# Performance work log

Measured on AMD Instinct MI355X. Metric: run time of the kernel, lower is better.

## Reference

```python
import jax, jax.numpy as jnp
import numpy as np

EPS = 1e-8


def setup_inputs() -> dict:
    key = jax.random.key(0)
    ks = jax.random.split(key, 8)
    B, N, D = 8, 2048, 768
    H, R = 768, 4
    return {
        "x": jax.random.normal(ks[0], (B, N, D), dtype=jnp.float32),
        "scale": jnp.ones((D,), dtype=jnp.float32),
        "U": jax.random.normal(ks[1], (H, R), dtype=jnp.float32) * 0.02,
        "V": jax.random.normal(ks[2], (H, R), dtype=jnp.float32) * 0.02,
        "S_param": jax.random.normal(ks[3], (H, H), dtype=jnp.float32) * 0.01,
        "Bm": jax.random.normal(ks[4], (H, D), dtype=jnp.float32) * (1.0 / np.sqrt(D)),
        "Cm": jax.random.normal(ks[5], (D, H), dtype=jnp.float32) * (1.0 / np.sqrt(H)),
        "gate_w": jax.random.normal(ks[6], (D, D), dtype=jnp.float32) * (1.0 / np.sqrt(D)),
        "gate_b": jnp.zeros((D,), dtype=jnp.float32),
        "alpha": jnp.full((1,), 0.1, dtype=jnp.float32),
    }


def reference(x, scale, U, V, S_param, Bm, Cm, gate_w, gate_b, alpha):
    B, N, D = x.shape
    H = Bm.shape[0]
    # A = diag(A_diag) + U V^T + (S - S^T); A_diag is a fixed buffer.
    A_diag = -jnp.linspace(1.0, float(H), H, dtype=x.dtype) / H
    A = jnp.diag(A_diag) + U @ V.T + (S_param - S_param.T)
    At = A.T  # apply as h @ A.T
    # RMSNorm
    rms = jnp.sqrt(jnp.mean(x * x, axis=-1, keepdims=True) + EPS)
    xn = x / rms * scale
    # Precompute input injections u_t = x_t @ B.T for all t: (N, B, H)
    u = jnp.einsum('bnd,hd->nbh', xn, Bm)

    def step(h, ut):
        h = h @ At + ut
        return h, h @ Cm.T  # (B, D)

    h0 = jnp.zeros((B, H), dtype=x.dtype)
    _, y_fwd = jax.lax.scan(step, h0, u)                 # (N, B, D)
    _, y_bwd = jax.lax.scan(step, h0, u, reverse=True)   # (N, B, D), indexed in time order
    y = 0.5 * (y_fwd + y_bwd)
    y = jnp.swapaxes(y, 0, 1)  # (B, N, D)
    # Gate
    g = jax.nn.sigmoid(jnp.einsum('bnd,ed->bne', xn, gate_w) + gate_b)
    y = y * g
    # Skip (dropout is identity in eval)
    return x + alpha * y
```

## Files before the change

kernel.cpp:

```cpp
#include <hip/hip_runtime.h>


typedef short  bfrag __attribute__((ext_vector_type(8)));
typedef float  ffrag __attribute__((ext_vector_type(4)));
typedef float  f4    __attribute__((ext_vector_type(4)));
typedef short  s4v   __attribute__((ext_vector_type(4)));

#define DEV static __device__ __forceinline__
#define Hn 768
#define FLS 132

DEV unsigned short f2bf(float f) {
  unsigned u = __float_as_uint(f);
  u += 0x7fffu + ((u >> 16) & 1u);
  return (unsigned short)(u >> 16);
}
DEV float bf2f(unsigned short s) { return __uint_as_float(((unsigned)s) << 16); }

DEV ffrag mfma16(bfrag a, bfrag b, ffrag c) {
  return __builtin_amdgcn_mfma_f32_16x16x32_bf16(a, b, c, 0, 0, 0);
}

DEV void glds16(const unsigned short* g, unsigned short* l) {
  __builtin_amdgcn_global_load_lds(
      (const __attribute__((address_space(1))) unsigned int*)g,
      (__attribute__((address_space(3))) unsigned int*)l, 16, 0, 0);
}

template<int N> DEV void vwait() {
  if constexpr (N == 0)       asm volatile("s_waitcnt vmcnt(0)" ::: "memory");
  else if constexpr (N == 4)  asm volatile("s_waitcnt vmcnt(4)" ::: "memory");
  else if constexpr (N == 6)  asm volatile("s_waitcnt vmcnt(6)" ::: "memory");
  else if constexpr (N == 8)  asm volatile("s_waitcnt vmcnt(8)" ::: "memory");
  else if constexpr (N == 12) asm volatile("s_waitcnt vmcnt(12)" ::: "memory");
}

union BF8 { bfrag v; unsigned short u[8]; };

__global__ __launch_bounds__(256) void k_abuild(
    const float* __restrict__ U, const float* __restrict__ V,
    const float* __restrict__ S, const float* __restrict__ Bm,
    const float* __restrict__ Cm, const float* __restrict__ gw,
    float* __restrict__ Af, float* __restrict__ AfT,
    unsigned short* __restrict__ Abf,
    unsigned short* __restrict__ Bmb, unsigned short* __restrict__ Cmb,
    unsigned short* __restrict__ gwb, unsigned short* __restrict__ zp) {
  int i = blockIdx.x;
  int task = blockIdx.y;
  if (task == 0) {
    float u0 = U[i*4+0], u1 = U[i*4+1], u2 = U[i*4+2], u3 = U[i*4+3];
    for (int j = threadIdx.x; j < Hn; j += 256) {
      float a = u0*V[j*4+0] + u1*V[j*4+1] + u2*V[j*4+2] + u3*V[j*4+3]
              + S[i*Hn+j] - S[j*Hn+i];
      if (i == j) a += -(float)(i+1) / 768.0f;
      Af[i*Hn+j]  = a;
      AfT[j*Hn+i] = a;
      Abf[i*Hn+j] = f2bf(a);
    }
    if (i == 0) for (int j = threadIdx.x; j < 1024; j += 256) zp[j] = 0;
  } else {
    const float* src = (task==1) ? Bm : (task==2) ? Cm : gw;
    unsigned short* dst = (task==1) ? Bmb : (task==2) ? Cmb : gwb;
    for (int j = threadIdx.x; j < Hn; j += 256) dst[i*Hn+j] = f2bf(src[i*Hn+j]);
  }
}

__global__ __launch_bounds__(256) void k_rms(
    const float* __restrict__ x, const float* __restrict__ scale,
    unsigned short* __restrict__ xn) {
  int row  = blockIdx.x * 4 + (threadIdx.x >> 6);
  int lane = threadIdx.x & 63;
  int b = row >> 11, t = row & 2047;
  const float* xr = x + (long)row * Hn;
  float v[12];
  float ss = 0.f;
#pragma unroll
  for (int j = 0; j < 12; ++j) { v[j] = xr[lane + j*64]; ss += v[j]*v[j]; }
#pragma unroll
  for (int off = 1; off < 64; off <<= 1) ss += __shfl_xor(ss, off);
  float inv = 1.0f / sqrtf(ss / 768.0f + 1e-8f);
  unsigned short* dst = xn + ((long)t * 8 + b) * Hn;
#pragma unroll
  for (int j = 0; j < 12; ++j) dst[lane + j*64] = f2bf(v[j] * inv * scale[lane + j*64]);
}

__global__ __launch_bounds__(512) void k_sq(
    const float* __restrict__ X, const float* __restrict__ XT,
    float* __restrict__ Z, float* __restrict__ ZT,
    unsigned short* __restrict__ Zbf) {
  int tid = threadIdx.x, lane = tid & 63, w = tid >> 6;
  int mw = w >> 2, nw = w & 3, l15 = lane & 15, lhi = lane >> 4;
  int rb = blockIdx.x * 64, cb = blockIdx.y * 128;
  ffrag acc[2][2] = {};
  for (int kt = 0; kt < 24; ++kt) {
    int k0 = kt*32 + lhi*8;
    BF8 ah[2], al[2], bh[2], bl[2];
#pragma unroll
    for (int mt = 0; mt < 2; ++mt) {
      const f4* p = (const f4*)(X + (long)(rb + mw*32 + mt*16 + l15) * Hn + k0);
      f4 x0 = p[0], x1 = p[1];
#pragma unroll
      for (int j = 0; j < 8; ++j) {
        float f = (j < 4) ? x0[j] : x1[j-4];
        unsigned short h = f2bf(f);
        ah[mt].u[j] = h; al[mt].u[j] = f2bf(f - bf2f(h));
      }
    }
#pragma unroll
    for (int nt = 0; nt < 2; ++nt) {
      const f4* p = (const f4*)(XT + (long)(cb + nw*32 + nt*16 + l15) * Hn + k0);
      f4 x0 = p[0], x1 = p[1];
#pragma unroll
      for (int j = 0; j < 8; ++j) {
        float f = (j < 4) ? x0[j] : x1[j-4];
        unsigned short h = f2bf(f);
        bh[nt].u[j] = h; bl[nt].u[j] = f2bf(f - bf2f(h));
      }
    }
#pragma unroll
    for (int mt = 0; mt < 2; ++mt)
#pragma unroll
      for (int nt = 0; nt < 2; ++nt) {
        acc[mt][nt] = mfma16(ah[mt].v, bh[nt].v, acc[mt][nt]);
        acc[mt][nt] = mfma16(ah[mt].v, bl[nt].v, acc[mt][nt]);
        acc[mt][nt] = mfma16(al[mt].v, bh[nt].v, acc[mt][nt]);
      }
  }
#pragma unroll
  for (int mt = 0; mt < 2; ++mt)
#pragma unroll
    for (int nt = 0; nt < 2; ++nt)
#pragma unroll
      for (int q = 0; q < 4; ++q) {
        int grow = rb + mw*32 + mt*16 + lhi*4 + q;
        int gcol = cb + nw*32 + nt*16 + l15;
        float vv = acc[mt][nt][q];
        Z[(long)grow*Hn + gcol] = vv;
        ZT[(long)gcol*Hn + grow] = vv;
        Zbf[(long)grow*Hn + gcol] = f2bf(vv);
      }
}

template<int MODE>
__global__ __launch_bounds__(256) void k_gemm(
    const unsigned short* __restrict__ A0s, const unsigned short* __restrict__ B0s,
    const unsigned short* __restrict__ res, unsigned short* __restrict__ outb,
    const unsigned short* __restrict__ zp, int sh, int dup,
    const unsigned short* __restrict__ yb,
    const float* __restrict__ gb, const float* __restrict__ alpha,
    const float* __restrict__ x, float* __restrict__ outf) {
  constexpr int NA   = (MODE == 1) ? 2 : 1;
  constexpr int NT   = NA + 1;
  constexpr int NBUF = (MODE == 1) ? 3 : 4;
  constexpr int LA   = NBUF - 1;
  constexpr int NL   = 2 * NT;

  __shared__ __align__(16) char smem[NBUF * NT * 8192];
  unsigned short* ldsb = (unsigned short*)smem;

  const int tid = threadIdx.x, lane = tid & 63, w = tid >> 6;
  const int l15 = lane & 15, lhi = lane >> 4;
  const int wr = w >> 1, wc = w & 1;

  const int nwg = gridDim.x;
  const int q8 = nwg >> 3, r8 = nwg & 7, xcd = blockIdx.x & 7, fo = blockIdx.x >> 3;
  const int wg = (xcd < r8 ? xcd*(q8+1) : r8*(q8+1) + (xcd - r8)*q8) + fo;
  const int cb = wg % 6, rbk = wg / 6;
  const long r0 = (long)rbk * 128;
  const long bc0 = (long)cb * 128;
  const int dir = (MODE == 0 && r0 >= 16384) ? 1 : 0;

  bool skip = false;
  if (MODE == 0 && sh > 0)
    skip = dir ? (r0 >= 32768 - sh) : (r0 + 128 <= sh);

  const int rowin = lane >> 2, ch = lane & 3;
  long gA[NA][2]; bool vA[NA][2]; long gB[2]; int lbase[2];
#pragma unroll
  for (int jj = 0; jj < 2; ++jj) {
    const int inst = w*2 + jj;
    const int r = inst*16 + rowin;
    const int c = ch ^ ((r ^ (r >> 2)) & 3);
    lbase[jj] = inst * 512;
#pragma unroll
    for (int s = 0; s < NA; ++s) {
      long gr; bool ok = true;
      if (MODE == 0) {
        gr = r0 + r + (dir ? sh : -sh);
        ok = dir ? (gr < 32768) : (gr >= 0);
      } else if (MODE == 1) {
        if (s == 0) { gr = r0 + r - sh; ok = (gr >= 0); }
        else        { gr = r0 + r + 16384 + sh; ok = (gr < 32768); }
      } else {
        gr = r0 + r;
      }
      vA[s][jj] = ok; gA[s][jj] = gr * Hn + c*8;
    }
    gB[jj] = (bc0 + r) * Hn + c*8;
  }

  auto stage = [&](int buf, int kt) {
    const int ko = kt * 32;
    unsigned short* dst = ldsb + buf * (NT * 4096);
#pragma unroll
    for (int jj = 0; jj < 2; ++jj) {
#pragma unroll
      for (int s = 0; s < NA; ++s) {
        const unsigned short* g = vA[s][jj] ? (A0s + gA[s][jj] + ko) : zp;
        glds16(g, dst + s*4096 + lbase[jj]);
      }
      glds16(B0s + gB[jj] + ko, dst + NA*4096 + lbase[jj]);
    }
  };

  ffrag acc[4][4] = {};
  const int cx = (lhi ^ ((l15 ^ (l15 >> 2)) & 3)) * 8;

  if (!skip) {
#pragma unroll
    for (int t = 0; t < LA; ++t) stage(t, t);
    int cur = 0, nb = LA;
    for (int kt = 0; kt < 24; ++kt) {
      const int rem = 23 - kt;
      if (rem >= LA - 1) vwait<NL * (LA - 1)>();
      else if (rem == 1) vwait<NL>();
      else               vwait<0>();
      __builtin_amdgcn_s_barrier();
      const unsigned short* L = ldsb + cur * (NT * 4096);
      bfrag a[NA][4], b[4];
#pragma unroll
      for (int mt = 0; mt < 4; ++mt) {
        const int row = wr*64 + mt*16 + l15;
#pragma unroll
        for (int s = 0; s < NA; ++s)
          a[s][mt] = *(const bfrag*)&L[s*4096 + row*32 + cx];
      }
#pragma unroll
      for (int nt = 0; nt < 4; ++nt) {
        const int row = wc*64 + nt*16 + l15;
        b[nt] = *(const bfrag*)&L[NA*4096 + row*32 + cx];
      }
#pragma unroll
      for (int mt = 0; mt < 4; ++mt)
#pragma unroll
        for (int nt = 0; nt < 4; ++nt) {
          acc[mt][nt] = mfma16(a[0][mt], b[nt], acc[mt][nt]);
          if (NA == 2) acc[mt][nt] = mfma16(a[1][mt], b[nt], acc[mt][nt]);
        }
      if (kt + LA <= 23) stage(nb, kt + LA);
      cur = (cur == NBUF-1) ? 0 : cur + 1;
      nb  = (nb  == NBUF-1) ? 0 : nb  + 1;
    }
  }

  float* fl = (float*)smem;
  const float al = (MODE == 2) ? alpha[0] : 0.f;
#pragma unroll
  for (int hh = 0; hh < 2; ++hh) {
    __syncthreads();
    if (wr == hh) {
#pragma unroll
      for (int mt = 0; mt < 4; ++mt)
#pragma unroll
        for (int nt = 0; nt < 4; ++nt)
#pragma unroll
          for (int q = 0; q < 4; ++q)
            fl[(mt*16 + lhi*4 + q)*FLS + wc*64 + nt*16 + l15] = acc[mt][nt][q];
    }
    __syncthreads();
    for (int i = tid; i < 2048; i += 256) {
      const int row = i >> 5;
      const int cc  = (i & 31) << 2;
      f4 v = *(const f4*)&fl[row*FLS + cc];
      const long grow = r0 + hh*64 + row;
      const long gcol = bc0 + cc;
      const long go = grow * Hn + gcol;
      if (MODE == 0) {
        if (res) {
          s4v rv = *(const s4v*)&res[go];
#pragma unroll
          for (int j = 0; j < 4; ++j) v[j] += bf2f(((unsigned short*)&rv)[j]);
        }
        s4v ov;
#pragma unroll
        for (int j = 0; j < 4; ++j) ((unsigned short*)&ov)[j] = f2bf(v[j]);
        *(s4v*)&outb[go] = ov;
        if (dup) *(s4v*)&outb[go + (long)16384*Hn] = ov;
      } else if (MODE == 1) {
        s4v ra = *(const s4v*)&res[go];
        s4v rb2 = *(const s4v*)&res[go + (long)16384*Hn];
#pragma unroll
        for (int j = 0; j < 4; ++j)
          v[j] += bf2f(((unsigned short*)&ra)[j]) + bf2f(((unsigned short*)&rb2)[j]);
        s4v ov;
#pragma unroll
        for (int j = 0; j < 4; ++j) ((unsigned short*)&ov)[j] = f2bf(v[j]);
        *(s4v*)&outb[go] = ov;
      } else {
        f4 gbv = *(const f4*)&gb[gcol];
        s4v yv = *(const s4v*)&yb[go];
        const long t = grow >> 3, b = grow & 7;
        const long o = (b*2048 + t)*Hn + gcol;
        f4 xv = *(const f4*)&x[o];
        f4 ov;
#pragma unroll
        for (int j = 0; j < 4; ++j) {
          float z = v[j] + gbv[j];
          float g = 1.0f / (1.0f + __expf(-z));
          ov[j] = xv[j] + al * 0.5f * bf2f(((unsigned short*)&yv)[j]) * g;
        }
        *(f4*)&outf[o] = ov;
      }
    }
  }
}

extern "C" void kernel_launch(void* const* d_in, const int* in_sizes, int n_in,
                              void* d_out, int out_size, void* d_ws, size_t ws_size,
                              hipStream_t stream) {
  const float* x     = (const float*)d_in[0];
  const float* scale = (const float*)d_in[1];
  const float* U     = (const float*)d_in[2];
  const float* V     = (const float*)d_in[3];
  const float* S     = (const float*)d_in[4];
  const float* Bm    = (const float*)d_in[5];
  const float* Cm    = (const float*)d_in[6];
  const float* gw    = (const float*)d_in[7];
  const float* gb    = (const float*)d_in[8];
  const float* alpha = (const float*)d_in[9];
  float* out = (float*)d_out;

  char* p = (char*)d_ws;
  auto alloc = [&](size_t sz) { char* r = p; p += (sz + 255) & ~(size_t)255; return r; };

  const size_t SZ_X  = (size_t)32768 * Hn * sizeof(unsigned short);
  const size_t SZ_BF = (size_t)16384 * Hn * sizeof(unsigned short);
  const size_t SZ_M  = (size_t)Hn * Hn * sizeof(float);
  const size_t SZ_MB = (size_t)Hn * Hn * sizeof(unsigned short);

  unsigned short* xn = (unsigned short*)alloc(SZ_BF);
  unsigned short* XA = (unsigned short*)alloc(SZ_X);
  unsigned short* XB = (unsigned short*)alloc(SZ_X);
  float* Af  = (float*)alloc(SZ_M);
  float* AfT = (float*)alloc(SZ_M);
  float* P1  = (float*)alloc(SZ_M);
  float* P1T = (float*)alloc(SZ_M);
  float* P2  = (float*)alloc(SZ_M);
  float* P2T = (float*)alloc(SZ_M);
  unsigned short* Abf = (unsigned short*)alloc(SZ_MB);
  unsigned short* Ab[10];
  for (int i = 0; i < 10; ++i) Ab[i] = (unsigned short*)alloc(SZ_MB);
  unsigned short* Bmb = (unsigned short*)alloc(SZ_MB);
  unsigned short* Cmb = (unsigned short*)alloc(SZ_MB);
  unsigned short* gwb = (unsigned short*)alloc(SZ_MB);
  unsigned short* zp  = (unsigned short*)alloc(1024 * sizeof(unsigned short));

  if ((size_t)(p - (char*)d_ws) > ws_size) return;

  k_abuild<<<dim3(768, 4), 256, 0, stream>>>(U, V, S, Bm, Cm, gw,
      Af, AfT, Abf, Bmb, Cmb, gwb, zp);
  k_rms<<<4096, 256, 0, stream>>>(x, scale, xn);

  const float* sx = Af; const float* sxt = AfT;
  float* za = P1; float* zat = P1T; float* zb = P2; float* zbt = P2T;
  for (int i = 0; i < 10; ++i) {
    k_sq<<<dim3(12, 6), 512, 0, stream>>>(sx, sxt, za, zat, Ab[i]);
    sx = za; sxt = zat;
    float* t1 = za; float* t2 = zat; za = zb; zat = zbt; zb = t1; zbt = t2;
  }

  k_gemm<0><<<768, 256, 0, stream>>>(xn, Bmb, nullptr, XA, zp, 0, 1,
      nullptr, nullptr, nullptr, nullptr, nullptr);

  unsigned short* src = XA; unsigned short* dst = XB;
  for (int i = 0; i < 10; ++i) {
    const unsigned short* W = (i == 0) ? Abf : Ab[i-1];
    k_gemm<0><<<1536, 256, 0, stream>>>(src, W, src, dst, zp, 8 << i, 0,
        nullptr, nullptr, nullptr, nullptr, nullptr);
    unsigned short* t = src; src = dst; dst = t;
  }
  k_gemm<1><<<768, 256, 0, stream>>>(src, Ab[9], src, XB, zp, 8192, 0,
      nullptr, nullptr, nullptr, nullptr, nullptr);

  unsigned short* ybuf = XB + (size_t)16384 * Hn;
  k_gemm<0><<<768, 256, 0, stream>>>(XB, Cmb, nullptr, ybuf, zp, 0, 0,
      nullptr, nullptr, nullptr, nullptr, nullptr);

  k_gemm<2><<<768, 256, 0, stream>>>(xn, gwb, nullptr, nullptr, zp, 0, 0,
      ybuf, gb, alpha, x, out);
}
```

Measured before the change: 1.311 ms.

## Fuse output projection GEMM with gate GEMM and rework LDS pipelining depth

```diff
diff --git a/kernel.cpp b/kernel.cpp
--- a/kernel.cpp
+++ b/kernel.cpp
@@ -28,11 +28,9 @@
 }
 
 template<int N> DEV void vwait() {
-  if constexpr (N == 0)       asm volatile("s_waitcnt vmcnt(0)" ::: "memory");
-  else if constexpr (N == 4)  asm volatile("s_waitcnt vmcnt(4)" ::: "memory");
-  else if constexpr (N == 6)  asm volatile("s_waitcnt vmcnt(6)" ::: "memory");
-  else if constexpr (N == 8)  asm volatile("s_waitcnt vmcnt(8)" ::: "memory");
-  else if constexpr (N == 12) asm volatile("s_waitcnt vmcnt(12)" ::: "memory");
+  if constexpr (N == 0)      asm volatile("s_waitcnt vmcnt(0)" ::: "memory");
+  else if constexpr (N == 4) asm volatile("s_waitcnt vmcnt(4)" ::: "memory");
+  else if constexpr (N == 8) asm volatile("s_waitcnt vmcnt(8)" ::: "memory");
 }
 
 union BF8 { bfrag v; unsigned short u[8]; };
@@ -143,16 +141,16 @@
 
 template<int MODE>
 __global__ __launch_bounds__(256) void k_gemm(
-    const unsigned short* __restrict__ A0s, const unsigned short* __restrict__ B0s,
+    const unsigned short* __restrict__ A0s, const unsigned short* __restrict__ A1s,
+    const unsigned short* __restrict__ B0s, const unsigned short* __restrict__ B1s,
     const unsigned short* __restrict__ res, unsigned short* __restrict__ outb,
     const unsigned short* __restrict__ zp, int sh, int dup,
-    const unsigned short* __restrict__ yb,
     const float* __restrict__ gb, const float* __restrict__ alpha,
     const float* __restrict__ x, float* __restrict__ outf) {
-  constexpr int NA   = (MODE == 1) ? 2 : 1;
-  constexpr int NT   = NA + 1;
-  constexpr int NBUF = (MODE == 1) ? 3 : 4;
-  constexpr int LA   = NBUF - 1;
+  constexpr int NA   = (MODE == 0) ? 1 : 2;
+  constexpr int NB   = (MODE == 2) ? 2 : 1;
+  constexpr int NT   = NA + NB;
+  constexpr int NBUF = (MODE == 0) ? 3 : 2;
   constexpr int NL   = 2 * NT;
 
   __shared__ __align__(16) char smem[NBUF * NT * 8192];
@@ -175,7 +173,7 @@
     skip = dir ? (r0 >= 32768 - sh) : (r0 + 128 <= sh);
 
   const int rowin = lane >> 2, ch = lane & 3;
-  long gA[NA][2]; bool vA[NA][2]; long gB[2]; int lbase[2];
+  long gA[NA][2]; bool vA[NA][2]; long gB[NB][2]; int lbase[2];
 #pragma unroll
   for (int jj = 0; jj < 2; ++jj) {
     const int inst = w*2 + jj;
@@ -196,7 +194,9 @@
       }
       vA[s][jj] = ok; gA[s][jj] = gr * Hn + c*8;
     }
-    gB[jj] = (bc0 + r) * Hn + c*8;
+#pragma unroll
+    for (int s = 0; s < NB; ++s)
+      gB[s][jj] = (bc0 + r) * Hn + c*8;
   }
 
   auto stage = [&](int buf, int kt) {
@@ -206,55 +206,101 @@
     for (int jj = 0; jj < 2; ++jj) {
 #pragma unroll
       for (int s = 0; s < NA; ++s) {
-        const unsigned short* g = vA[s][jj] ? (A0s + gA[s][jj] + ko) : zp;
+        const unsigned short* src0 = (MODE == 2 && s == 1) ? A1s : A0s;
+        const unsigned short* g = vA[s][jj] ? (src0 + gA[s][jj] + ko) : zp;
         glds16(g, dst + s*4096 + lbase[jj]);
       }
-      glds16(B0s + gB[jj] + ko, dst + NA*4096 + lbase[jj]);
+#pragma unroll
+      for (int s = 0; s < NB; ++s) {
+        const unsigned short* src0 = (s == 0) ? B0s : B1s;
+        glds16(src0 + gB[s][jj] + ko, dst + (NA + s)*4096 + lbase[jj]);
+      }
     }
   };
 
   ffrag acc[4][4] = {};
+  ffrag accZ[(MODE == 2) ? 4 : 1][(MODE == 2) ? 4 : 1] = {};
   const int cx = (lhi ^ ((l15 ^ (l15 >> 2)) & 3)) * 8;
 
   if (!skip) {
-#pragma unroll
-    for (int t = 0; t < LA; ++t) stage(t, t);
-    int cur = 0, nb = LA;
-    for (int kt = 0; kt < 24; ++kt) {
-      const int rem = 23 - kt;
-      if (rem >= LA - 1) vwait<NL * (LA - 1)>();
-      else if (rem == 1) vwait<NL>();
-      else               vwait<0>();
-      __builtin_amdgcn_s_barrier();
-      const unsigned short* L = ldsb + cur * (NT * 4096);
-      bfrag a[NA][4], b[4];
-#pragma unroll
-      for (int mt = 0; mt < 4; ++mt) {
-        const int row = wr*64 + mt*16 + l15;
-#pragma unroll
-        for (int s = 0; s < NA; ++s)
-          a[s][mt] = *(const bfrag*)&L[s*4096 + row*32 + cx];
-      }
-#pragma unroll
-      for (int nt = 0; nt < 4; ++nt) {
-        const int row = wc*64 + nt*16 + l15;
-        b[nt] = *(const bfrag*)&L[NA*4096 + row*32 + cx];
-      }
-#pragma unroll
-      for (int mt = 0; mt < 4; ++mt)
+    if (MODE == 0) {
+      stage(0, 0); stage(1, 1);
+      int cur = 0;
+      for (int kt = 0; kt < 24; ++kt) {
+        if (kt < 23) vwait<4>(); else vwait<0>();
+        __builtin_amdgcn_s_barrier();
+        if (kt + 2 <= 23) stage((kt + 2) % 3, kt + 2);
+        const unsigned short* L = ldsb + cur * (NT * 4096);
+        bfrag a0[4], b0[4];
+#pragma unroll
+        for (int mt = 0; mt < 4; ++mt)
+          a0[mt] = *(const bfrag*)&L[(wr*64 + mt*16 + l15)*32 + cx];
+#pragma unroll
+        for (int nt = 0; nt < 4; ++nt)
+          b0[nt] = *(const bfrag*)&L[4096 + (wc*64 + nt*16 + l15)*32 + cx];
+#pragma unroll
+        for (int mt = 0; mt < 4; ++mt)
+#pragma unroll
+          for (int nt = 0; nt < 4; ++nt)
+            acc[mt][nt] = mfma16(a0[mt], b0[nt], acc[mt][nt]);
+        cur = (cur == 2) ? 0 : cur + 1;
+      }
+    } else {
+      stage(0, 0);
+      int cur = 0;
+      for (int kt = 0; kt < 24; ++kt) {
+        vwait<0>();
+        __builtin_amdgcn_s_barrier();
+        if (kt < 23) stage(cur ^ 1, kt + 1);
+        const unsigned short* L = ldsb + cur * (NT * 4096);
+        bfrag a[2][4], b0[4], b1[4];
+#pragma unroll
+        for (int mt = 0; mt < 4; ++mt) {
+          const int row = wr*64 + mt*16 + l15;
+          a[0][mt] = *(const bfrag*)&L[row*32 + cx];
+          a[1][mt] = *(const bfrag*)&L[4096 + row*32 + cx];
+        }
 #pragma unroll
         for (int nt = 0; nt < 4; ++nt) {
-          acc[mt][nt] = mfma16(a[0][mt], b[nt], acc[mt][nt]);
-          if (NA == 2) acc[mt][nt] = mfma16(a[1][mt], b[nt], acc[mt][nt]);
+          const int row = wc*64 + nt*16 + l15;
+          b0[nt] = *(const bfrag*)&L[2*4096 + row*32 + cx];
+          if (MODE == 2) b1[nt] = *(const bfrag*)&L[3*4096 + row*32 + cx];
         }
-      if (kt + LA <= 23) stage(nb, kt + LA);
-      cur = (cur == NBUF-1) ? 0 : cur + 1;
-      nb  = (nb  == NBUF-1) ? 0 : nb  + 1;
-    }
+#pragma unroll
+        for (int mt = 0; mt < 4; ++mt)
+#pragma unroll
+          for (int nt = 0; nt < 4; ++nt) {
+            if (MODE == 1) {
+              acc[mt][nt] = mfma16(a[0][mt], b0[nt], acc[mt][nt]);
+              acc[mt][nt] = mfma16(a[1][mt], b0[nt], acc[mt][nt]);
+            } else {
+              acc[mt][nt]  = mfma16(a[0][mt], b0[nt], acc[mt][nt]);
+              accZ[mt][nt] = mfma16(a[1][mt], b1[nt], accZ[mt][nt]);
+            }
+          }
+        cur ^= 1;
+      }
+    }
+  }
+
+  if (MODE == 2) {
+    const float al = alpha[0];
+    float gvals[4];
+#pragma unroll
+    for (int nt = 0; nt < 4; ++nt) gvals[nt] = gb[bc0 + wc*64 + nt*16 + l15];
+#pragma unroll
+    for (int mt = 0; mt < 4; ++mt)
+#pragma unroll
+      for (int nt = 0; nt < 4; ++nt)
+#pragma unroll
+        for (int q = 0; q < 4; ++q) {
+          float z = accZ[mt][nt][q] + gvals[nt];
+          float g = 1.0f / (1.0f + __expf(-z));
+          acc[mt][nt][q] *= al * 0.5f * g;
+        }
   }
 
   float* fl = (float*)smem;
-  const float al = (MODE == 2) ? alpha[0] : 0.f;
 #pragma unroll
   for (int hh = 0; hh < 2; ++hh) {
     __syncthreads();
@@ -297,18 +343,12 @@
         for (int j = 0; j < 4; ++j) ((unsigned short*)&ov)[j] = f2bf(v[j]);
         *(s4v*)&outb[go] = ov;
       } else {
-        f4 gbv = *(const f4*)&gb[gcol];
-        s4v yv = *(const s4v*)&yb[go];
         const long t = grow >> 3, b = grow & 7;
         const long o = (b*2048 + t)*Hn + gcol;
         f4 xv = *(const f4*)&x[o];
         f4 ov;
 #pragma unroll
-        for (int j = 0; j < 4; ++j) {
-          float z = v[j] + gbv[j];
-          float g = 1.0f / (1.0f + __expf(-z));
-          ov[j] = xv[j] + al * 0.5f * bf2f(((unsigned short*)&yv)[j]) * g;
-        }
+        for (int j = 0; j < 4; ++j) ov[j] = xv[j] + v[j];
         *(f4*)&outf[o] = ov;
       }
     }
@@ -369,23 +409,20 @@
     float* t1 = za; float* t2 = zat; za = zb; zat = zbt; zb = t1; zbt = t2;
   }
 
-  k_gemm<0><<<768, 256, 0, stream>>>(xn, Bmb, nullptr, XA, zp, 0, 1,
-      nullptr, nullptr, nullptr, nullptr, nullptr);
+  k_gemm<0><<<768, 256, 0, stream>>>(xn, nullptr, Bmb, nullptr, nullptr, XA,
+      zp, 0, 1, nullptr, nullptr, nullptr, nullptr);
 
   unsigned short* src = XA; unsigned short* dst = XB;
   for (int i = 0; i < 10; ++i) {
     const unsigned short* W = (i == 0) ? Abf : Ab[i-1];
-    k_gemm<0><<<1536, 256, 0, stream>>>(src, W, src, dst, zp, 8 << i, 0,
-        nullptr, nullptr, nullptr, nullptr, nullptr);
+    k_gemm<0><<<1536, 256, 0, stream>>>(src, nullptr, W, nullptr, src, dst,
+        zp, 8 << i, 0, nullptr, nullptr, nullptr, nullptr);
     unsigned short* t = src; src = dst; dst = t;
   }
-  k_gemm<1><<<768, 256, 0, stream>>>(src, Ab[9], src, XB, zp, 8192, 0,
-      nullptr, nullptr, nullptr, nullptr, nullptr);
-
-  unsigned short* ybuf = XB + (size_t)16384 * Hn;
-  k_gemm<0><<<768, 256, 0, stream>>>(XB, Cmb, nullptr, ybuf, zp, 0, 0,
-      nullptr, nullptr, nullptr, nullptr, nullptr);
-
-  k_gemm<2><<<768, 256, 0, stream>>>(xn, gwb, nullptr, nullptr, zp, 0, 0,
-      ybuf, gb, alpha, x, out);
-}
+  unsigned short* xsum = (src == XA) ? XB : XA;
+  k_gemm<1><<<768, 256, 0, stream>>>(src, nullptr, Ab[9], nullptr, src, xsum,
+      zp, 8192, 0, nullptr, nullptr, nullptr, nullptr);
+
+  k_gemm<2><<<768, 256, 0, stream>>>(xsum, xn, Cmb, gwb, nullptr, nullptr,
+      zp, 0, 0, gb, alpha, x, out);
+}
```

New measurement: 1.262 ms. 1.04x faster.
